# Performance work log

Hardware: AMD Instinct MI355X
Metric: run time of the kernel (lower is better)

## Reference

```python
import jax, jax.numpy as jnp
import numpy as np

B, N, NIMP = 65536, 256, 128
FAR = 1e10


def _compute_weights(deltas, density, eps=1e-10):
    # deltas, density: [B, P]
    ep = jnp.exp(-density * deltas)                     # exp(-sigma*delta)
    T = jnp.cumprod(
        jnp.concatenate([jnp.ones_like(ep[:, :1]), ep], axis=1)[:, :-1], axis=1
    )                                                   # transmittance [B, P]
    return T * (1.0 - ep) + eps


def _deltas(z):
    return jnp.concatenate([z[..., 1:] - z[..., :-1],
                            jnp.full_like(z[..., :1], FAR)], axis=-1)


def _sample_pdf(bins, weights, u):
    # bins: [B, Nb], weights: [B, Nb-1], u: [B, Ns]
    weights = weights + 1e-5
    pdf = weights / jnp.sum(weights, axis=-1, keepdims=True)
    cdf = jnp.cumsum(pdf, axis=-1)
    cdf = jnp.concatenate([jnp.zeros_like(cdf[..., :1]), cdf], axis=-1)  # [B, Nb]
    inds = jax.vmap(lambda c, uu: jnp.searchsorted(c, uu, side='right'))(cdf, u)
    below = jnp.maximum(inds - 1, 0)
    above = jnp.minimum(inds, cdf.shape[-1] - 1)
    cdf_b = jnp.take_along_axis(cdf, below, axis=-1)
    cdf_a = jnp.take_along_axis(cdf, above, axis=-1)
    bins_b = jnp.take_along_axis(bins, below, axis=-1)
    bins_a = jnp.take_along_axis(bins, above, axis=-1)
    denom = cdf_a - cdf_b
    denom = jnp.where(denom < 1e-5, jnp.ones_like(denom), denom)
    t = (u - cdf_b) / denom
    return bins_b + t * (bins_a - bins_b)


def setup_inputs() -> dict:
    key = jax.random.key(0)
    ks = jax.random.split(key, 6)
    z_vals = jnp.sort(jax.random.uniform(ks[0], (B, N), jnp.float32, 2.0, 6.0), axis=-1)
    density = jax.random.uniform(ks[1], (B, N), jnp.float32) * 2.0
    feature = jax.random.uniform(ks[2], (B, N, 3), jnp.float32)
    fine_density = jax.random.uniform(ks[3], (B, N + NIMP), jnp.float32) * 2.0
    fine_feature = jax.random.uniform(ks[4], (B, N + NIMP, 3), jnp.float32)
    u_rand = jax.random.uniform(ks[5], (B, NIMP), jnp.float32)
    return {"z_vals": z_vals, "density": density, "feature": feature,
            "fine_density": fine_density, "fine_feature": fine_feature,
            "u_rand": u_rand}


def reference(z_vals, density, feature, fine_density, fine_feature, u_rand):
    # ---- coarse pass ----
    w = _compute_weights(_deltas(z_vals), density)            # [B, N]
    feat = jnp.sum(w[..., None] * feature, axis=1)            # [B, 3]
    depth = jnp.sum(w * z_vals, axis=-1, keepdims=True)       # [B, 1]
    # ---- importance sampling (detached in original) ----
    z_mid = 0.5 * (z_vals[..., 1:] + z_vals[..., :-1])        # [B, N-1]
    z_samples = jax.lax.stop_gradient(
        _sample_pdf(z_mid, w[..., 1:-1], u_rand))             # [B, NIMP]
    z_fine = jnp.sort(jnp.concatenate([z_vals, z_samples], axis=-1), axis=-1)
    # ---- fine pass ----
    wf = _compute_weights(_deltas(z_fine), fine_density)      # [B, N+NIMP]
    fine_feat = jnp.sum(wf[..., None] * fine_feature, axis=1)  # [B, 3]
    fine_depth = jnp.sum(wf * z_fine, axis=-1, keepdims=True)  # [B, 1]
    return jnp.concatenate([feat, depth, fine_feat, fine_depth], axis=-1)  # [B, 8]
```

## Files before the change

### kernel.cpp

```cpp
#include <hip/hip_runtime.h>
#include <cstdint>

#define FARV 1e10f

constexpr int NC  = 256;
constexpr int NS  = 128;
constexpr int NF  = 384;
constexpr int RPB = 4;

__device__ __forceinline__ float wave_incl_scan_prod(float v, int lane) {
  float x = v;
#pragma unroll
  for (int off = 1; off < 64; off <<= 1) {
    float o = __shfl_up(x, off);
    if (lane >= off) x *= o;
  }
  return x;
}

__device__ __forceinline__ float wave_incl_scan_add(float v, int lane) {
  float x = v;
#pragma unroll
  for (int off = 1; off < 64; off <<= 1) {
    float o = __shfl_up(x, off);
    if (lane >= off) x += o;
  }
  return x;
}

__device__ __forceinline__ int wave_incl_scan_addi(int v, int lane) {
  int x = v;
#pragma unroll
  for (int off = 1; off < 64; off <<= 1) {
    int o = __shfl_up(x, off);
    if (lane >= off) x += o;
  }
  return x;
}

__device__ __forceinline__ float wave_reduce(float v) {
#pragma unroll
  for (int off = 32; off; off >>= 1) v += __shfl_down(v, off);
  return v;
}

__device__ __forceinline__ int upper_bound_lds(const float* arr, int n, float u) {
  int lo = 0;
  while (n > 0) {
    int h = n >> 1;
    int mid = lo + h;
    if (arr[mid] <= u) { lo = mid + 1; n -= h + 1; }
    else n = h;
  }
  return lo;
}

__device__ __forceinline__ void cmpswap_local(float& a, float& b, bool asc) {
  const float lo = fminf(a, b), hi = fmaxf(a, b);
  a = asc ? lo : hi;
  b = asc ? hi : lo;
}

__device__ __forceinline__ float cmpswap_xor(float v, int m, bool take_min) {
  const float p = __shfl_xor(v, m);
  return take_min ? fminf(v, p) : fmaxf(v, p);
}

__device__ __forceinline__ void bitonic_sort128(float& v0, float& v1, int lane) {
  {
    const bool asc = ((lane & 1) == 0);
    cmpswap_local(v0, v1, asc);
  }
#pragma unroll
  for (int k = 4; k <= 128; k <<= 1) {
    const int kh = k >> 1;
    const bool asc = ((lane & kh) == 0);
#pragma unroll
    for (int j = kh; j >= 2; j >>= 1) {
      const int m = j >> 1;
      const bool take_min = (((lane & m) == 0) == asc);
      v0 = cmpswap_xor(v0, m, take_min);
      v1 = cmpswap_xor(v1, m, take_min);
    }
    cmpswap_local(v0, v1, asc);
  }
}

__global__ __launch_bounds__(256, 8) void vr_kernel(
    const float* __restrict__ z_vals,
    const float* __restrict__ density,
    const float* __restrict__ feature,
    const float* __restrict__ fine_density,
    const float* __restrict__ fine_feature,
    const float* __restrict__ u_rand,
    float* __restrict__ out)
{
  __shared__ __align__(16) float zv[RPB][NC];
  __shared__ __align__(16) float cdfs[RPB][NC];
  __shared__ __align__(16) int   Hh[RPB][NC];
  __shared__ __align__(16) float zf[RPB][NF];

  const int wid  = threadIdx.x >> 6;
  const int lane = threadIdx.x & 63;
  const int ray  = blockIdx.x * RPB + wid;

  *(int4*)(&Hh[wid][lane * 4]) = make_int4(0, 0, 0, 0);

  const float2 uu = *(const float2*)(u_rand + (size_t)ray * NS + lane * 2);

  const float4 z4 = *(const float4*)(z_vals  + (size_t)ray * NC + lane * 4);
  const float4 d4 = *(const float4*)(density + (size_t)ray * NC + lane * 4);
  const float4 fA = *(const float4*)(feature + (size_t)ray * NC * 3 + lane * 12);
  const float4 fB = *(const float4*)(feature + (size_t)ray * NC * 3 + lane * 12 + 4);
  const float4 fC = *(const float4*)(feature + (size_t)ray * NC * 3 + lane * 12 + 8);

  *(float4*)(&zv[wid][lane * 4]) = z4;

  const float znext = __shfl_down(z4.x, 1);
  const float dl0 = z4.y - z4.x;
  const float dl1 = z4.z - z4.y;
  const float dl2 = z4.w - z4.z;
  const float dl3 = (lane == 63) ? FARV : (znext - z4.w);

  const float e0 = __expf(-d4.x * dl0);
  const float e1 = __expf(-d4.y * dl1);
  const float e2 = __expf(-d4.z * dl2);
  const float e3 = __expf(-d4.w * dl3);

  const float p1 = e0, p2 = e0 * e1, p3 = p2 * e2, ptot = p3 * e3;
  const float incl = wave_incl_scan_prod(ptot, lane);
  float Tb = __shfl_up(incl, 1);
  if (lane == 0) Tb = 1.0f;

  const float w0 = Tb *      (1.0f - e0) + 1e-10f;
  const float w1 = Tb * p1 * (1.0f - e1) + 1e-10f;
  const float w2 = Tb * p2 * (1.0f - e2) + 1e-10f;
  const float w3 = Tb * p3 * (1.0f - e3) + 1e-10f;

  float fx = w0 * fA.x + w1 * fA.w + w2 * fB.z + w3 * fC.y;
  float fy = w0 * fA.y + w1 * fB.x + w2 * fB.w + w3 * fC.z;
  float fz = w0 * fA.z + w1 * fB.y + w2 * fC.x + w3 * fC.w;
  float dep = w0 * z4.x + w1 * z4.y + w2 * z4.z + w3 * z4.w;

  const float wn0 = __shfl_down(w0, 1);
  const bool l63 = (lane == 63);
  const float m0 = w1 + 1e-5f;
  const float m1 = w2 + 1e-5f;
  const float m2 = l63 ? 0.0f : (w3 + 1e-5f);
  const float m3 = l63 ? 0.0f : (wn0 + 1e-5f);
  const float c1 = m0 + m1;
  const float c2 = c1 + m2;
  const float c3 = c2 + m3;
  const float inclS = wave_incl_scan_add(c3, lane);
  float Sb = __shfl_up(inclS, 1);
  if (lane == 0) Sb = 0.0f;
  const float total = __shfl(inclS, 63);
  const float inv = 1.0f / total;

  cdfs[wid][4 * lane + 1] = (Sb + m0) * inv;
  cdfs[wid][4 * lane + 2] = (Sb + c1) * inv;
  if (!l63) {
    cdfs[wid][4 * lane + 3] = (Sb + c2) * inv;
    cdfs[wid][4 * lane + 4] = (Sb + c3) * inv;
  }
  if (lane == 0) cdfs[wid][0] = 0.0f;

  float v0 = uu.x, v1 = uu.y;
  bitonic_sort128(v0, v1, lane);

  __syncthreads();

#pragma unroll
  for (int t = 0; t < 2; ++t) {
    const float u = t ? v1 : v0;
    const int ind = upper_bound_lds(&cdfs[wid][0], 255, u);
    const int below = (ind > 0) ? ind - 1 : 0;
    const int above = (ind < 254) ? ind : 254;
    const float cb = cdfs[wid][below];
    const float ca = cdfs[wid][above];
    const float zb0 = zv[wid][below];
    const float zb1 = zv[wid][below + 1];
    const float zb2 = zv[wid][(below + 2 < 256) ? below + 2 : 255];
    const float bb = 0.5f * (zb0 + zb1);
    const float ba = 0.5f * (zb1 + zb2);
    float den = ca - cb;
    den = (den < 1e-5f) ? 1.0f : den;
    const float tt = (u - cb) / den;
    const float s = bb + tt * (ba - bb);
    int u_ = below + 1 + ((s >= zb1) ? 1 : 0) + ((s >= zb2) ? 1 : 0);
    const int up = (u_ > 255) ? 255 : u_;
    atomicAdd(&Hh[wid][up], 1);
    zf[wid][up + 2 * lane + t] = s;
  }

  __syncthreads();

  const int4 h4 = *(const int4*)(&Hh[wid][4 * lane]);
  const int t0 = h4.x;
  const int t1 = t0 + h4.y;
  const int t2 = t1 + h4.z;
  const int t3 = t2 + h4.w;
  const int inclH = wave_incl_scan_addi(t3, lane);
  int Hb = __shfl_up(inclH, 1);
  if (lane == 0) Hb = 0;

  zf[wid][4 * lane + 0 + Hb + t0] = z4.x;
  zf[wid][4 * lane + 1 + Hb + t1] = z4.y;
  zf[wid][4 * lane + 2 + Hb + t2] = z4.z;
  zf[wid][4 * lane + 3 + Hb + t3] = z4.w;

  __syncthreads();

  const int p0 = 6 * lane;
  const float* zfp = &zf[wid][p0];
  const float2 zp0 = *(const float2*)(zfp);
  const float2 zp1 = *(const float2*)(zfp + 2);
  const float2 zp2 = *(const float2*)(zfp + 4);
  float zq[7];
  zq[0] = zp0.x; zq[1] = zp0.y; zq[2] = zp1.x; zq[3] = zp1.y;
  zq[4] = zp2.x; zq[5] = zp2.y;
  zq[6] = (lane < 63) ? zfp[6] : 0.0f;

  float dlf[6];
#pragma unroll
  for (int j = 0; j < 5; ++j) dlf[j] = zq[j + 1] - zq[j];
  dlf[5] = (lane == 63) ? FARV : (zq[6] - zq[5]);

  const float* fd = fine_density + (size_t)ray * NF + p0;
  const float2 q0 = *(const float2*)(fd);
  const float2 q1 = *(const float2*)(fd + 2);
  const float2 q2 = *(const float2*)(fd + 4);
  const float fdv[6] = {q0.x, q0.y, q1.x, q1.y, q2.x, q2.y};

  float ee[6];
#pragma unroll
  for (int j = 0; j < 6; ++j) ee[j] = __expf(-fdv[j] * dlf[j]);

  float P[6];
  P[0] = 1.0f;
#pragma unroll
  for (int j = 1; j < 6; ++j) P[j] = P[j - 1] * ee[j - 1];
  const float ftot = P[5] * ee[5];

  const float incF = wave_incl_scan_prod(ftot, lane);
  float Tb2 = __shfl_up(incF, 1);
  if (lane == 0) Tb2 = 1.0f;

  float wfv[6];
  float fdep = 0.0f;
#pragma unroll
  for (int j = 0; j < 6; ++j) {
    wfv[j] = Tb2 * P[j] * (1.0f - ee[j]) + 1e-10f;
    fdep += wfv[j] * zq[j];
  }

  float* wfp = &zf[wid][p0];
  *(float2*)(wfp)     = make_float2(wfv[0], wfv[1]);
  *(float2*)(wfp + 2) = make_float2(wfv[2], wfv[3]);
  *(float2*)(wfp + 4) = make_float2(wfv[4], wfv[5]);

  __syncthreads();

  float gx = 0.0f, gy = 0.0f, gz = 0.0f;
  const float* ffb = fine_feature + (size_t)ray * (NF * 3);
#pragma unroll
  for (int r = 0; r < 6; ++r) {
    const int idx = r * 64 + lane;
    const float w = zf[wid][idx];
    const float* fp = ffb + idx * 3;
    gx += w * fp[0];
    gy += w * fp[1];
    gz += w * fp[2];
  }

  fx = wave_reduce(fx);
  fy = wave_reduce(fy);
  fz = wave_reduce(fz);
  dep = wave_reduce(dep);
  gx = wave_reduce(gx);
  gy = wave_reduce(gy);
  gz = wave_reduce(gz);
  fdep = wave_reduce(fdep);

  if (lane == 0) {
    float* o = out + (size_t)ray * 8;
    *(float4*)(o)     = make_float4(fx, fy, fz, dep);
    *(float4*)(o + 4) = make_float4(gx, gy, gz, fdep);
  }
}

extern "C" void kernel_launch(void* const* d_in, const int* in_sizes, int n_in,
                              void* d_out, int out_size, void* d_ws, size_t ws_size,
                              hipStream_t stream) {
  const float* z_vals       = (const float*)d_in[0];
  const float* density      = (const float*)d_in[1];
  const float* feature      = (const float*)d_in[2];
  const float* fine_density = (const float*)d_in[3];
  const float* fine_feature = (const float*)d_in[4];
  const float* u_rand       = (const float*)d_in[5];
  float* out = (float*)d_out;

  const int B = in_sizes[0] / NC;
  dim3 grid(B / RPB), block(RPB * 64);
  hipLaunchKernelGGL(vr_kernel, grid, block, 0, stream,
                     z_vals, density, feature, fine_density, fine_feature,
                     u_rand, out);
}
```

Before: 142.4 us.

## Use DPP wave scans, drop block barriers, two-level CDF search, padded LDS

```diff
diff --git a/kernel.cpp b/kernel.cpp
--- a/kernel.cpp
+++ b/kernel.cpp
@@ -7,53 +7,58 @@
 constexpr int NS  = 128;
 constexpr int NF  = 384;
 constexpr int RPB = 4;
-
-__device__ __forceinline__ float wave_incl_scan_prod(float v, int lane) {
-  float x = v;
-#pragma unroll
-  for (int off = 1; off < 64; off <<= 1) {
-    float o = __shfl_up(x, off);
-    if (lane >= off) x *= o;
-  }
+constexpr int ZFP = 400;
+
+template<int CTRL, int RM, int BM>
+__device__ __forceinline__ float dppf(float old, float x) {
+  return __int_as_float(__builtin_amdgcn_update_dpp(
+      __float_as_int(old), __float_as_int(x), CTRL, RM, BM, false));
+}
+template<int CTRL, int RM, int BM>
+__device__ __forceinline__ int dppi(int old, int x) {
+  return __builtin_amdgcn_update_dpp(old, x, CTRL, RM, BM, false);
+}
+template<int CTRL>
+__device__ __forceinline__ float dppq(float x) {
+  return __int_as_float(__builtin_amdgcn_update_dpp(
+      0, __float_as_int(x), CTRL, 0xf, 0xf, true));
+}
+template<int MASK>
+__device__ __forceinline__ float swzx(float x) {
+  return __int_as_float(__builtin_amdgcn_ds_swizzle(
+      __float_as_int(x), (MASK << 10) | 0x1f));
+}
+
+__device__ __forceinline__ float scan_incl_mul(float x) {
+  x *= dppf<0x111, 0xf, 0xf>(1.f, x);
+  x *= dppf<0x112, 0xf, 0xf>(1.f, x);
+  x *= dppf<0x114, 0xf, 0xf>(1.f, x);
+  x *= dppf<0x118, 0xf, 0xf>(1.f, x);
+  x *= dppf<0x142, 0xa, 0xf>(1.f, x);
+  x *= dppf<0x143, 0xc, 0xf>(1.f, x);
   return x;
 }
-
-__device__ __forceinline__ float wave_incl_scan_add(float v, int lane) {
-  float x = v;
-#pragma unroll
-  for (int off = 1; off < 64; off <<= 1) {
-    float o = __shfl_up(x, off);
-    if (lane >= off) x += o;
-  }
+__device__ __forceinline__ float scan_incl_add(float x) {
+  x += dppf<0x111, 0xf, 0xf>(0.f, x);
+  x += dppf<0x112, 0xf, 0xf>(0.f, x);
+  x += dppf<0x114, 0xf, 0xf>(0.f, x);
+  x += dppf<0x118, 0xf, 0xf>(0.f, x);
+  x += dppf<0x142, 0xa, 0xf>(0.f, x);
+  x += dppf<0x143, 0xc, 0xf>(0.f, x);
   return x;
 }
-
-__device__ __forceinline__ int wave_incl_scan_addi(int v, int lane) {
-  int x = v;
-#pragma unroll
-  for (int off = 1; off < 64; off <<= 1) {
-    int o = __shfl_up(x, off);
-    if (lane >= off) x += o;
-  }
+__device__ __forceinline__ int scan_incl_addi(int x) {
+  x += dppi<0x111, 0xf, 0xf>(0, x);
+  x += dppi<0x112, 0xf, 0xf>(0, x);
+  x += dppi<0x114, 0xf, 0xf>(0, x);
+  x += dppi<0x118, 0xf, 0xf>(0, x);
+  x += dppi<0x142, 0xa, 0xf>(0, x);
+  x += dppi<0x143, 0xc, 0xf>(0, x);
   return x;
 }
-
-__device__ __forceinline__ float wave_reduce(float v) {
-#pragma unroll
-  for (int off = 32; off; off >>= 1) v += __shfl_down(v, off);
-  return v;
-}
-
-__device__ __forceinline__ int upper_bound_lds(const float* arr, int n, float u) {
-  int lo = 0;
-  while (n > 0) {
-    int h = n >> 1;
-    int mid = lo + h;
-    if (arr[mid] <= u) { lo = mid + 1; n -= h + 1; }
-    else n = h;
-  }
-  return lo;
-}
+__device__ __forceinline__ float wshr1(float x, float id) { return dppf<0x138, 0xf, 0xf>(id, x); }
+__device__ __forceinline__ int   wshr1i(int x)            { return dppi<0x138, 0xf, 0xf>(0, x); }
+__device__ __forceinline__ float wshl1(float x)           { return dppf<0x130, 0xf, 0xf>(0.f, x); }
 
 __device__ __forceinline__ void cmpswap_local(float& a, float& b, bool asc) {
   const float lo = fminf(a, b), hi = fmaxf(a, b);
@@ -61,29 +66,36 @@
   b = asc ? hi : lo;
 }
 
-__device__ __forceinline__ float cmpswap_xor(float v, int m, bool take_min) {
-  const float p = __shfl_xor(v, m);
-  return take_min ? fminf(v, p) : fmaxf(v, p);
-}
-
+template<int M>
+__device__ __forceinline__ float xpartner(float v) {
+  if constexpr (M == 1)       return dppq<0xB1>(v);
+  else if constexpr (M == 2)  return dppq<0x4E>(v);
+  else if constexpr (M <= 16) return swzx<M>(v);
+  else                        return __shfl_xor(v, M);
+}
+template<int M>
+__device__ __forceinline__ void merge_down(float& v0, float& v1, bool asc, int lane) {
+  const bool tm = ((lane & M) == 0) == asc;
+  const float p0 = xpartner<M>(v0);
+  const float p1 = xpartner<M>(v1);
+  v0 = tm ? fminf(v0, p0) : fmaxf(v0, p0);
+  v1 = tm ? fminf(v1, p1) : fmaxf(v1, p1);
+  if constexpr (M > 1) merge_down<M / 2>(v0, v1, asc, lane);
+}
+template<int K>
+__device__ __forceinline__ void bitonic_stage(float& v0, float& v1, int lane) {
+  const bool asc = (lane & (K >> 1)) == 0;
+  merge_down<K / 4>(v0, v1, asc, lane);
+  cmpswap_local(v0, v1, asc);
+}
 __device__ __forceinline__ void bitonic_sort128(float& v0, float& v1, int lane) {
-  {
-    const bool asc = ((lane & 1) == 0);
-    cmpswap_local(v0, v1, asc);
-  }
-#pragma unroll
-  for (int k = 4; k <= 128; k <<= 1) {
-    const int kh = k >> 1;
-    const bool asc = ((lane & kh) == 0);
-#pragma unroll
-    for (int j = kh; j >= 2; j >>= 1) {
-      const int m = j >> 1;
-      const bool take_min = (((lane & m) == 0) == asc);
-      v0 = cmpswap_xor(v0, m, take_min);
-      v1 = cmpswap_xor(v1, m, take_min);
-    }
-    cmpswap_local(v0, v1, asc);
-  }
+  cmpswap_local(v0, v1, (lane & 1) == 0);
+  bitonic_stage<4>(v0, v1, lane);
+  bitonic_stage<8>(v0, v1, lane);
+  bitonic_stage<16>(v0, v1, lane);
+  bitonic_stage<32>(v0, v1, lane);
+  bitonic_stage<64>(v0, v1, lane);
+  bitonic_stage<128>(v0, v1, lane);
 }
 
 __global__ __launch_bounds__(256, 8) void vr_kernel(
@@ -97,12 +109,15 @@
 {
   __shared__ __align__(16) float zv[RPB][NC];
   __shared__ __align__(16) float cdfs[RPB][NC];
+  __shared__ __align__(16) float cdfg[RPB][64];
   __shared__ __align__(16) int   Hh[RPB][NC];
-  __shared__ __align__(16) float zf[RPB][NF];
+  __shared__ __align__(16) float zf[RPB][ZFP];
 
   const int wid  = threadIdx.x >> 6;
   const int lane = threadIdx.x & 63;
   const int ray  = blockIdx.x * RPB + wid;
+
+  float* const zfr = &zf[wid][0];
 
   *(int4*)(&Hh[wid][lane * 4]) = make_int4(0, 0, 0, 0);
 
@@ -116,7 +131,7 @@
 
   *(float4*)(&zv[wid][lane * 4]) = z4;
 
-  const float znext = __shfl_down(z4.x, 1);
+  const float znext = wshl1(z4.x);
   const float dl0 = z4.y - z4.x;
   const float dl1 = z4.z - z4.y;
   const float dl2 = z4.w - z4.z;
@@ -128,9 +143,8 @@
   const float e3 = __expf(-d4.w * dl3);
 
   const float p1 = e0, p2 = e0 * e1, p3 = p2 * e2, ptot = p3 * e3;
-  const float incl = wave_incl_scan_prod(ptot, lane);
-  float Tb = __shfl_up(incl, 1);
-  if (lane == 0) Tb = 1.0f;
+  const float incl = scan_incl_mul(ptot);
+  const float Tb = wshr1(incl, 1.0f);
 
   const float w0 = Tb *      (1.0f - e0) + 1e-10f;
   const float w1 = Tb * p1 * (1.0f - e1) + 1e-10f;
@@ -142,7 +156,7 @@
   float fz = w0 * fA.z + w1 * fB.y + w2 * fC.x + w3 * fC.w;
   float dep = w0 * z4.x + w1 * z4.y + w2 * z4.z + w3 * z4.w;
 
-  const float wn0 = __shfl_down(w0, 1);
+  const float wn0 = wshl1(w0);
   const bool l63 = (lane == 63);
   const float m0 = w1 + 1e-5f;
   const float m1 = w2 + 1e-5f;
@@ -151,33 +165,36 @@
   const float c1 = m0 + m1;
   const float c2 = c1 + m2;
   const float c3 = c2 + m3;
-  const float inclS = wave_incl_scan_add(c3, lane);
-  float Sb = __shfl_up(inclS, 1);
-  if (lane == 0) Sb = 0.0f;
-  const float total = __shfl(inclS, 63);
+  const float inclS = scan_incl_add(c3);
+  const float Sb = wshr1(inclS, 0.0f);
+  const float total = __int_as_float(__builtin_amdgcn_readlane(__float_as_int(inclS), 63));
   const float inv = 1.0f / total;
 
-  cdfs[wid][4 * lane + 1] = (Sb + m0) * inv;
-  cdfs[wid][4 * lane + 2] = (Sb + c1) * inv;
-  if (!l63) {
-    cdfs[wid][4 * lane + 3] = (Sb + c2) * inv;
-    cdfs[wid][4 * lane + 4] = (Sb + c3) * inv;
-  }
-  if (lane == 0) cdfs[wid][0] = 0.0f;
+  *(float4*)(&cdfs[wid][4 * lane]) =
+      make_float4(Sb * inv, (Sb + m0) * inv, (Sb + c1) * inv, (Sb + c2) * inv);
+  cdfg[wid][lane] = Sb * inv;
 
   float v0 = uu.x, v1 = uu.y;
   bitonic_sort128(v0, v1, lane);
 
-  __syncthreads();
-
 #pragma unroll
   for (int t = 0; t < 2; ++t) {
     const float u = t ? v1 : v0;
-    const int ind = upper_bound_lds(&cdfs[wid][0], 255, u);
-    const int below = (ind > 0) ? ind - 1 : 0;
-    const int above = (ind < 254) ? ind : 254;
-    const float cb = cdfs[wid][below];
-    const float ca = cdfs[wid][above];
+    int g = 0;
+#pragma unroll
+    for (int st = 32; st; st >>= 1) {
+      const int cand = g + st;
+      if (cdfg[wid][cand] <= u) g = cand;
+    }
+    const float4 f4 = *(const float4*)(&cdfs[wid][4 * g]);
+    const float nxt = cdfs[wid][(4 * g + 4 < 256) ? 4 * g + 4 : 255];
+    const int ind = 4 * g + 1 + ((u >= f4.y) ? 1 : 0) + ((u >= f4.z) ? 1 : 0)
+                              + ((u >= f4.w) ? 1 : 0);
+    const int below = ind - 1;
+    const int r = ind - 4 * g;
+    const float cb = (r == 1) ? f4.x : (r == 2) ? f4.y : (r == 3) ? f4.z : f4.w;
+    float ca = (r == 1) ? f4.y : (r == 2) ? f4.z : (r == 3) ? f4.w : nxt;
+    if (ind > 254) ca = f4.z;
     const float zb0 = zv[wid][below];
     const float zb1 = zv[wid][below + 1];
     const float zb2 = zv[wid][(below + 2 < 256) ? below + 2 : 255];
@@ -190,36 +207,38 @@
     int u_ = below + 1 + ((s >= zb1) ? 1 : 0) + ((s >= zb2) ? 1 : 0);
     const int up = (u_ > 255) ? 255 : u_;
     atomicAdd(&Hh[wid][up], 1);
-    zf[wid][up + 2 * lane + t] = s;
-  }
-
-  __syncthreads();
+    const int si = up + 2 * lane + t;
+    zfr[si + (si >> 5)] = s;
+  }
 
   const int4 h4 = *(const int4*)(&Hh[wid][4 * lane]);
   const int t0 = h4.x;
   const int t1 = t0 + h4.y;
   const int t2 = t1 + h4.z;
   const int t3 = t2 + h4.w;
-  const int inclH = wave_incl_scan_addi(t3, lane);
-  int Hb = __shfl_up(inclH, 1);
-  if (lane == 0) Hb = 0;
-
-  zf[wid][4 * lane + 0 + Hb + t0] = z4.x;
-  zf[wid][4 * lane + 1 + Hb + t1] = z4.y;
-  zf[wid][4 * lane + 2 + Hb + t2] = z4.z;
-  zf[wid][4 * lane + 3 + Hb + t3] = z4.w;
-
-  __syncthreads();
+  const int inclH = scan_incl_addi(t3);
+  const int Hb = wshr1i(inclH);
+
+  {
+    const int i0 = 4 * lane + 0 + Hb + t0;
+    const int i1 = 4 * lane + 1 + Hb + t1;
+    const int i2 = 4 * lane + 2 + Hb + t2;
+    const int i3 = 4 * lane + 3 + Hb + t3;
+    zfr[i0 + (i0 >> 5)] = z4.x;
+    zfr[i1 + (i1 >> 5)] = z4.y;
+    zfr[i2 + (i2 >> 5)] = z4.z;
+    zfr[i3 + (i3 >> 5)] = z4.w;
+  }
 
   const int p0 = 6 * lane;
-  const float* zfp = &zf[wid][p0];
-  const float2 zp0 = *(const float2*)(zfp);
-  const float2 zp1 = *(const float2*)(zfp + 2);
-  const float2 zp2 = *(const float2*)(zfp + 4);
   float zq[7];
-  zq[0] = zp0.x; zq[1] = zp0.y; zq[2] = zp1.x; zq[3] = zp1.y;
-  zq[4] = zp2.x; zq[5] = zp2.y;
-  zq[6] = (lane < 63) ? zfp[6] : 0.0f;
+  {
+    const float2 a = *(const float2*)(zfr + p0     + (p0 >> 5));
+    const float2 b = *(const float2*)(zfr + p0 + 2 + ((p0 + 2) >> 5));
+    const float2 c = *(const float2*)(zfr + p0 + 4 + ((p0 + 4) >> 5));
+    zq[0] = a.x; zq[1] = a.y; zq[2] = b.x; zq[3] = b.y; zq[4] = c.x; zq[5] = c.y;
+    zq[6] = (lane < 63) ? zfr[p0 + 6 + ((p0 + 6) >> 5)] : 0.0f;
+  }
 
   float dlf[6];
 #pragma unroll
@@ -242,9 +261,8 @@
   for (int j = 1; j < 6; ++j) P[j] = P[j - 1] * ee[j - 1];
   const float ftot = P[5] * ee[5];
 
-  const float incF = wave_incl_scan_prod(ftot, lane);
-  float Tb2 = __shfl_up(incF, 1);
-  if (lane == 0) Tb2 = 1.0f;
+  const float incF = scan_incl_mul(ftot);
+  const float Tb2 = wshr1(incF, 1.0f);
 
   float wfv[6];
   float fdep = 0.0f;
@@ -254,35 +272,43 @@
     fdep += wfv[j] * zq[j];
   }
 
-  float* wfp = &zf[wid][p0];
-  *(float2*)(wfp)     = make_float2(wfv[0], wfv[1]);
-  *(float2*)(wfp + 2) = make_float2(wfv[2], wfv[3]);
-  *(float2*)(wfp + 4) = make_float2(wfv[4], wfv[5]);
-
-  __syncthreads();
-
-  float gx = 0.0f, gy = 0.0f, gz = 0.0f;
-  const float* ffb = fine_feature + (size_t)ray * (NF * 3);
-#pragma unroll
-  for (int r = 0; r < 6; ++r) {
-    const int idx = r * 64 + lane;
-    const float w = zf[wid][idx];
-    const float* fp = ffb + idx * 3;
-    gx += w * fp[0];
-    gy += w * fp[1];
-    gz += w * fp[2];
-  }
-
-  fx = wave_reduce(fx);
-  fy = wave_reduce(fy);
-  fz = wave_reduce(fz);
-  dep = wave_reduce(dep);
-  gx = wave_reduce(gx);
-  gy = wave_reduce(gy);
-  gz = wave_reduce(gz);
-  fdep = wave_reduce(fdep);
-
-  if (lane == 0) {
+  __builtin_amdgcn_sched_barrier(0);
+
+  zfr[p0 + 0] = wfv[0];
+  zfr[p0 + 1] = wfv[1];
+  zfr[p0 + 2] = wfv[2];
+  zfr[p0 + 3] = wfv[3];
+  zfr[p0 + 4] = wfv[4];
+  zfr[p0 + 5] = wfv[5];
+
+  const float4 wq = *(const float4*)(zfr + 4 * lane);
+  const float* fb = fine_feature + (size_t)ray * (NF * 3) + lane * 12;
+  const float4 ga = *(const float4*)(fb);
+  const float4 gb = *(const float4*)(fb + 4);
+  const float4 gc = *(const float4*)(fb + 8);
+  float gx = wq.x * ga.x + wq.y * ga.w + wq.z * gb.z + wq.w * gc.y;
+  float gy = wq.x * ga.y + wq.y * gb.x + wq.z * gb.w + wq.w * gc.z;
+  float gz = wq.x * ga.z + wq.y * gb.y + wq.z * gc.x + wq.w * gc.w;
+
+  const float2 wt2 = *(const float2*)(zfr + 256 + 2 * lane);
+  const float* fb2 = fine_feature + (size_t)ray * (NF * 3) + 768 + lane * 6;
+  const float2 qa = *(const float2*)(fb2);
+  const float2 qb = *(const float2*)(fb2 + 2);
+  const float2 qc = *(const float2*)(fb2 + 4);
+  gx += wt2.x * qa.x + wt2.y * qb.y;
+  gy += wt2.x * qa.y + wt2.y * qc.x;
+  gz += wt2.x * qb.x + wt2.y * qc.y;
+
+  fx   = scan_incl_add(fx);
+  fy   = scan_incl_add(fy);
+  fz   = scan_incl_add(fz);
+  dep  = scan_incl_add(dep);
+  gx   = scan_incl_add(gx);
+  gy   = scan_incl_add(gy);
+  gz   = scan_incl_add(gz);
+  fdep = scan_incl_add(fdep);
+
+  if (lane == 63) {
     float* o = out + (size_t)ray * 8;
     *(float4*)(o)     = make_float4(fx, fy, fz, dep);
     *(float4*)(o + 4) = make_float4(gx, gy, gz, fdep);
```

New measurement: 129.0 us. 9.4% less time.
